# Kernel tuning notes

Measured on AMD Instinct MI355X. Metric: run time of the kernel, lower is better.

## Reference

```python
import jax, jax.numpy as jnp
import numpy as np

D_MODEL = 1024
NUM_HEADS = 16
THETA = 10000.0
BATCH = 2
SEQ = 2048


def _rope(x, pos, theta):
    # x: (b, h, l, d), pos: (l,)
    d = x.shape[-1]
    half = d // 2
    inv_freq = theta ** (-(jnp.arange(half, dtype=x.dtype) / half))  # theta^(-2k/d)
    ang = pos.astype(x.dtype)[:, None] * inv_freq[None, :]  # (l, half)
    cos, sin = jnp.cos(ang), jnp.sin(ang)
    x1, x2 = x[..., ::2], x[..., 1::2]
    r1 = x1 * cos - x2 * sin
    r2 = x1 * sin + x2 * cos
    return jnp.stack([r1, r2], axis=-1).reshape(x.shape)


def setup_inputs() -> dict:
    key = jax.random.key(0)
    k1, k2, k3 = jax.random.split(key, 3)
    x = jax.random.normal(k1, (BATCH, SEQ, D_MODEL), dtype=jnp.float32)
    W_kqv = jax.random.normal(k2, (3 * D_MODEL, D_MODEL), dtype=jnp.float32) * (1.0 / np.sqrt(D_MODEL))
    W_o = jax.random.normal(k3, (D_MODEL, D_MODEL), dtype=jnp.float32) * (1.0 / np.sqrt(D_MODEL))
    return {"x": x, "W_kqv": W_kqv, "W_o": W_o}


def reference(x, W_kqv, W_o):
    b, L, _ = x.shape
    h = NUM_HEADS
    d = D_MODEL // h
    kqv = x @ W_kqv.T  # (b, l, 3*d_model)
    K, Q, V = jnp.split(kqv, 3, axis=-1)  # chunk order in source: K, Q, V
    # (b, l, h*d) -> (b, h, l, d)
    Q = Q.reshape(b, L, h, d).transpose(0, 2, 1, 3)
    K = K.reshape(b, L, h, d).transpose(0, 2, 1, 3)
    V = V.reshape(b, L, h, d).transpose(0, 2, 1, 3)
    pos = jnp.arange(L)
    Q = _rope(Q, pos, THETA)
    K = _rope(K, pos, THETA)
    scores = jnp.einsum('bhqd,bhkd->bhqk', Q, K) / jnp.sqrt(jnp.asarray(d, x.dtype))
    causal = jnp.tril(jnp.ones((L, L), dtype=bool))
    scores = jnp.where(causal, scores, jnp.finfo(scores.dtype).min)
    probs = jax.nn.softmax(scores, axis=-1)
    out = jnp.einsum('bhqk,bhkd->bhqd', probs, V)
    out = out.transpose(0, 2, 1, 3).reshape(b, L, h * d)
    return out @ W_o.T
```

## Files before the change

kernel.cpp:

```cpp
#include <hip/hip_runtime.h>
#include <hip/hip_bf16.h>
#include <stdint.h>

#define BATCH 2
#define SEQ 2048
#define DMODEL 1024
#define NHEADS 16
#define HDIM 64
#define MROWS (BATCH*SEQ)
#define N3 (3*DMODEL)

typedef __attribute__((ext_vector_type(8))) __bf16 bf16x8;
typedef __attribute__((ext_vector_type(4))) float f32x4;

__device__ __forceinline__ ushort f2b(float f) {
  uint32_t u = __builtin_bit_cast(uint32_t, f);
  uint32_t r = (u + 0x7FFFu + ((u >> 16) & 1u)) >> 16;
  return (ushort)r;
}
__device__ __forceinline__ float b2f(ushort h) {
  return __builtin_bit_cast(float, (uint32_t)h << 16);
}
__device__ __forceinline__ float exp2_hw(float x) {
  float r;
  asm("v_exp_f32 %0, %1" : "=v"(r) : "v"(x));
  return r;
}
__device__ __forceinline__ uint32_t cvtpk(float a, float b) {
  uint32_t r;
  asm("v_cvt_pk_bf16_f32 %0, %1, %2" : "=v"(r) : "v"(a), "v"(b));
  return r;
}

__global__ void f2b3_kernel(const float* __restrict__ a, const float* __restrict__ b,
                            const float* __restrict__ c,
                            ushort* __restrict__ oa, ushort* __restrict__ ob,
                            ushort* __restrict__ oc, int na, int nb, int nc) {
  int i = blockIdx.x * blockDim.x + threadIdx.x;
  const float* src; ushort* dst; int off;
  if (i < na)           { src = a; dst = oa; off = i; }
  else if (i < na + nb) { src = b; dst = ob; off = i - na; }
  else if (i < na + nb + nc) { src = c; dst = oc; off = i - na - nb; }
  else return;
  float4 v = ((const float4*)src)[off];
  uint32_t lo = cvtpk(v.x, v.y), hi_ = cvtpk(v.z, v.w);
  ((uint2*)dst)[off] = make_uint2(lo, hi_);
}

template<int OUTF>
__global__ __launch_bounds__(256)
void gemm_bt(const ushort* __restrict__ A, const ushort* __restrict__ Bw,
             void* __restrict__ Cv, int M, int N, int K) {
  __shared__ __align__(16) ushort As[128*64];
  __shared__ __align__(16) ushort Bs[128*64];
  const int tid  = threadIdx.x;
  const int wid  = tid >> 6;
  const int lane = tid & 63;
  const int wr   = wid >> 1, wc = wid & 1;
  const int l16  = lane & 15, lhi = lane >> 4;
  const int nb   = N >> 7;
  const int brow = (blockIdx.x / nb) << 7;
  const int bcol = (blockIdx.x % nb) << 7;

  f32x4 acc[4][4] = {};

  for (int k0 = 0; k0 < K; k0 += 64) {
    __syncthreads();
#pragma unroll
    for (int it = 0; it < 4; ++it) {
      const int cb = (wid * 4 + it) * 64;
      const int ci = cb + lane;
      const int r  = ci >> 3;
      const int sl = (ci & 7) ^ (r & 7);
      const ushort* ga = A  + (size_t)(brow + r) * K + k0 + sl * 8;
      const ushort* gb = Bw + (size_t)(bcol + r) * K + k0 + sl * 8;
      __builtin_amdgcn_global_load_lds(
          (const __attribute__((address_space(1))) void*)ga,
          (__attribute__((address_space(3))) void*)(As + cb * 8), 16, 0, 0);
      __builtin_amdgcn_global_load_lds(
          (const __attribute__((address_space(1))) void*)gb,
          (__attribute__((address_space(3))) void*)(Bs + cb * 8), 16, 0, 0);
    }
    __syncthreads();

#pragma unroll
    for (int kk = 0; kk < 2; ++kk) {
      bf16x8 af[4], bfr[4];
#pragma unroll
      for (int m = 0; m < 4; ++m)
        af[m] = *(const bf16x8*)(As + (wr*64 + m*16 + l16)*64 + (((kk*4+lhi) ^ (l16 & 7)) * 8));
#pragma unroll
      for (int n = 0; n < 4; ++n)
        bfr[n] = *(const bf16x8*)(Bs + (wc*64 + n*16 + l16)*64 + (((kk*4+lhi) ^ (l16 & 7)) * 8));
#pragma unroll
      for (int m = 0; m < 4; ++m)
#pragma unroll
        for (int n = 0; n < 4; ++n)
          acc[m][n] = __builtin_amdgcn_mfma_f32_16x16x32_bf16(af[m], bfr[n], acc[m][n], 0, 0, 0);
    }
  }

#pragma unroll
  for (int m = 0; m < 4; ++m)
#pragma unroll
    for (int n = 0; n < 4; ++n)
#pragma unroll
      for (int r = 0; r < 4; ++r) {
        const int row = brow + wr*64 + m*16 + lhi*4 + r;
        const int col = bcol + wc*64 + n*16 + l16;
        if (OUTF) ((float*)Cv)[(size_t)row * N + col] = acc[m][n][r];
        else      ((ushort*)Cv)[(size_t)row * N + col] = f2b(acc[m][n][r]);
      }
}

__global__ __launch_bounds__(256)
void prep_kernel(const ushort* __restrict__ kqv,
                 ushort* __restrict__ qb, ushort* __restrict__ kb, ushort* __restrict__ vt) {
  __shared__ ushort tile[64][65];
  if (blockIdx.x < 1024) {
    int bid = blockIdx.x;
    int lt = bid & 31, bh = bid >> 5;
    int b = bh >> 4, h = bh & 15;
    int tid = threadIdx.x;
    int r = tid >> 2, cq = tid & 3;
    size_t gbase = ((size_t)(b * SEQ + lt * 64 + r)) * N3 + 2 * DMODEL + h * HDIM + cq * 16;
#pragma unroll
    for (int j = 0; j < 16; ++j) tile[r][cq * 16 + j] = kqv[gbase + j];
    __syncthreads();
    int d = tid >> 2;
    size_t obase = ((size_t)(bh * HDIM + d)) * SEQ + lt * 64 + cq * 16;
#pragma unroll
    for (int j = 0; j < 16; ++j) vt[obase + j] = tile[cq * 16 + j][d];
  } else {
    const float SC = 0.18033688011112042f;
    int idx = (blockIdx.x - 1024) * 256 + threadIdx.x;
    int i  = idx & 31;
    int h  = (idx >> 5) & 15;
    int bl = idx >> 9;
    int l  = bl & (SEQ - 1);
    int b  = bl >> 11;
    float inv = exp2f((float)i * -0.4152410118609203f);
    float ang = (float)l * inv;
    float s, c;
    sincosf(ang, &s, &c);
    size_t base = (size_t)bl * N3 + h * HDIM + 2 * i;
    uint32_t kp = *(const uint32_t*)(kqv + base);
    uint32_t qp = *(const uint32_t*)(kqv + base + DMODEL);
    float k1 = b2f((ushort)(kp & 0xffff)), k2 = b2f((ushort)(kp >> 16));
    float q1 = b2f((ushort)(qp & 0xffff)), q2 = b2f((ushort)(qp >> 16));
    float kr1 = k1 * c - k2 * s, kr2 = k1 * s + k2 * c;
    float qr1 = (q1 * c - q2 * s) * SC, qr2 = (q1 * s + q2 * c) * SC;
    size_t ob = ((size_t)(b * NHEADS + h) * SEQ + l) * HDIM + 2 * i;
    *(uint32_t*)(kb + ob) = cvtpk(kr1, kr2);
    *(uint32_t*)(qb + ob) = cvtpk(qr1, qr2);
  }
}

__global__ __launch_bounds__(256, 2)
void attn_kernel(const ushort* __restrict__ qb, const ushort* __restrict__ kb,
                 const ushort* __restrict__ vt, ushort* __restrict__ ao) {
  __shared__ __align__(16) ushort Kbuf[3][4096];
  __shared__ __align__(16) ushort Vbuf[3][4096];
  __shared__ __align__(16) ushort plds[4][1024];
  const int bid = blockIdx.x;
  const int bh = bid & 31;
  const int p  = bid >> 5;
  const int qtA = p, qtB = 31 - p;

  const int wid = threadIdx.x >> 6, lane = threadIdx.x & 63;
  const int l16 = lane & 15, lhi = lane >> 4;
  const int r0A = qtA * 64 + wid * 16;
  const int r0B = qtB * 64 + wid * 16;

  const ushort* Q  = qb + (size_t)bh * SEQ * HDIM;
  const ushort* Kp = kb + (size_t)bh * SEQ * HDIM;
  const ushort* Vp = vt + (size_t)bh * HDIM * SEQ;

  bf16x8 qfA[2], qfB[2];
#pragma unroll
  for (int kc = 0; kc < 2; ++kc) {
    qfA[kc] = *(const bf16x8*)(Q + (size_t)(r0A + l16) * HDIM + kc * 32 + lhi * 8);
    qfB[kc] = *(const bf16x8*)(Q + (size_t)(r0B + l16) * HDIM + kc * 32 + lhi * 8);
  }

  float mqA = -3.0e38f, lsA = 0.0f, mqB = -3.0e38f, lsB = 0.0f;
  f32x4 oA[4] = {}, oB[4] = {};

  char* pbase = (char*)&plds[wid][0];
  const int swz = (l16 & 7) << 4;

  auto STAGE = [&](int buf, int kt) {
    ushort* kd = &Kbuf[buf][0];
    ushort* vd = &Vbuf[buf][0];
    const ushort* kg = Kp + (size_t)kt * 64 * HDIM;
    const ushort* vg = Vp + kt * 64;
#pragma unroll
    for (int it = 0; it < 2; ++it) {
      const int cb = it * 256 + wid * 64;
      const int ci = cb + lane;
      const int row = ci >> 3;
      const int sl  = (ci & 7) ^ (row & 7);
      __builtin_amdgcn_global_load_lds(
          (const __attribute__((address_space(1))) void*)(kg + row * HDIM + sl * 8),
          (__attribute__((address_space(3))) void*)(kd + cb * 8), 16, 0, 0);
      __builtin_amdgcn_global_load_lds(
          (const __attribute__((address_space(1))) void*)(vg + (size_t)row * SEQ + sl * 8),
          (__attribute__((address_space(3))) void*)(vd + cb * 8), 16, 0, 0);
    }
  };

  auto BODY = [&](const char* kc_, const char* vc_, bf16x8 (&qf)[2],
                  float& mq, float& lsq, f32x4 (&o)[4], int r0, int qt, int kt) {
    f32x4 s[4];
#pragma unroll
    for (int n = 0; n < 4; ++n) {
      const int kvr = n * 16 + l16;
      bf16x8 kf0 = *(const bf16x8*)(kc_ + kvr*128 + ((lhi     ^ (kvr&7)) * 16));
      bf16x8 kf1 = *(const bf16x8*)(kc_ + kvr*128 + (((4+lhi) ^ (kvr&7)) * 16));
      f32x4 z = 0.0f;
      z = __builtin_amdgcn_mfma_f32_16x16x32_bf16(kf0, qf[0], z, 0, 0, 0);
      z = __builtin_amdgcn_mfma_f32_16x16x32_bf16(kf1, qf[1], z, 0, 0, 0);
      s[n] = z;
    }
    if (kt == qt) {
#pragma unroll
      for (int n = 0; n < 4; ++n)
#pragma unroll
        for (int r = 0; r < 4; ++r)
          if (kt*64 + n*16 + lhi*4 + r > r0 + l16) s[n][r] = -3.0e38f;
    }
    float t0 = fmaxf(fmaxf(s[0][0], s[0][1]), fmaxf(s[0][2], s[0][3]));
    float t1 = fmaxf(fmaxf(s[1][0], s[1][1]), fmaxf(s[1][2], s[1][3]));
    float t2 = fmaxf(fmaxf(s[2][0], s[2][1]), fmaxf(s[2][2], s[2][3]));
    float t3 = fmaxf(fmaxf(s[3][0], s[3][1]), fmaxf(s[3][2], s[3][3]));
    float pmx = fmaxf(fmaxf(t0, t1), fmaxf(t2, t3));
    pmx = fmaxf(pmx, __shfl_xor(pmx, 16));
    pmx = fmaxf(pmx, __shfl_xor(pmx, 32));

    if (!__all(pmx <= mq)) {
      float mn = fmaxf(mq, pmx);
      float alpha = exp2_hw(mq - mn);
      mq = mn;
      lsq *= alpha;
      float alphaT[4];
#pragma unroll
      for (int r = 0; r < 4; ++r)
        alphaT[r] = __shfl(alpha, lhi * 4 + r);
#pragma unroll
      for (int f = 0; f < 4; ++f)
#pragma unroll
        for (int r = 0; r < 4; ++r)
          o[f][r] *= alphaT[r];
    }

    float ps = 0.0f;
#pragma unroll
    for (int n = 0; n < 4; ++n)
#pragma unroll
      for (int r = 0; r < 4; ++r) {
        float pv = exp2_hw(s[n][r] - mq);
        s[n][r] = pv;
        ps += pv;
      }
    ps += __shfl_xor(ps, 16);
    ps += __shfl_xor(ps, 32);
    lsq += ps;

#pragma unroll
    for (int n = 0; n < 4; ++n) {
      uint32_t w0 = cvtpk(s[n][0], s[n][1]);
      uint32_t w1 = cvtpk(s[n][2], s[n][3]);
      int kvloc = n*16 + lhi*4;
      *(uint32_t*)(pbase + ((l16*128 + kvloc*2) ^ swz))       = w0;
      *(uint32_t*)(pbase + ((l16*128 + (kvloc+2)*2) ^ swz))   = w1;
    }
    bf16x8 pa0 = *(const bf16x8*)(pbase + ((l16*128 + 0*64 + lhi*16) ^ swz));
    bf16x8 pa1 = *(const bf16x8*)(pbase + ((l16*128 + 1*64 + lhi*16) ^ swz));

#pragma unroll
    for (int f = 0; f < 4; ++f) {
      const int dr = f * 16 + l16;
      bf16x8 vf0 = *(const bf16x8*)(vc_ + dr*128 + ((lhi     ^ (dr&7)) * 16));
      bf16x8 vf1 = *(const bf16x8*)(vc_ + dr*128 + (((4+lhi) ^ (dr&7)) * 16));
      o[f] = __builtin_amdgcn_mfma_f32_16x16x32_bf16(pa0, vf0, o[f], 0, 0, 0);
      o[f] = __builtin_amdgcn_mfma_f32_16x16x32_bf16(pa1, vf1, o[f], 0, 0, 0);
    }
  };

  STAGE(0, 0);
  STAGE(1, 1);

  for (int kt = 0; kt <= qtB; ++kt) {
    if (kt < qtB) asm volatile("s_waitcnt vmcnt(4)" ::: "memory");
    else          asm volatile("s_waitcnt vmcnt(0)" ::: "memory");
    __builtin_amdgcn_s_barrier();
    __builtin_amdgcn_sched_barrier(0);

    if (kt + 2 <= qtB) STAGE((kt + 2) % 3, kt + 2);

    const char* kc_ = (const char*)&Kbuf[kt % 3][0];
    const char* vc_ = (const char*)&Vbuf[kt % 3][0];
    BODY(kc_, vc_, qfB, mqB, lsB, oB, r0B, qtB, kt);
    if (kt <= qtA)
      BODY(kc_, vc_, qfA, mqA, lsA, oA, r0A, qtA, kt);

    __builtin_amdgcn_sched_barrier(0);
  }

  const int b = bh >> 4, h = bh & 15;
  float invA = 1.0f / lsA, invB = 1.0f / lsB;
#pragma unroll
  for (int r = 0; r < 4; ++r) {
    float wA = __shfl(invA, lhi * 4 + r);
    float wB = __shfl(invB, lhi * 4 + r);
    size_t baseA = ((size_t)(b * SEQ + r0A + lhi*4 + r)) * DMODEL + h * HDIM + l16;
    size_t baseB = ((size_t)(b * SEQ + r0B + lhi*4 + r)) * DMODEL + h * HDIM + l16;
#pragma unroll
    for (int f = 0; f < 4; ++f) {
      ao[baseA + f*16] = f2b(oA[f][r] * wA);
      ao[baseB + f*16] = f2b(oB[f][r] * wB);
    }
  }
}

extern "C" void kernel_launch(void* const* d_in, const int* in_sizes, int n_in,
                              void* d_out, int out_size, void* d_ws, size_t ws_size,
                              hipStream_t stream) {
  const float* x    = (const float*)d_in[0];
  const float* wkqv = (const float*)d_in[1];
  const float* wo   = (const float*)d_in[2];
  float* out = (float*)d_out;

  ushort* xb   = (ushort*)d_ws;
  ushort* wkb  = xb  + (size_t)MROWS * DMODEL;
  ushort* wob  = wkb + (size_t)N3 * DMODEL;
  ushort* kqv  = wob + (size_t)DMODEL * DMODEL;
  ushort* qb   = kqv + (size_t)MROWS * N3;
  ushort* kb   = qb  + (size_t)MROWS * DMODEL;
  ushort* vt   = kb  + (size_t)MROWS * DMODEL;
  ushort* attn = xb;

  int nx = MROWS * DMODEL / 4, nw = N3 * DMODEL / 4, no = DMODEL * DMODEL / 4;
  f2b3_kernel<<<(nx + nw + no) / 256, 256, 0, stream>>>(x, wkqv, wo, xb, wkb, wob, nx, nw, no);

  gemm_bt<0><<<(MROWS/128) * (N3/128), 256, 0, stream>>>(xb, wkb, (void*)kqv, MROWS, N3, DMODEL);

  prep_kernel<<<1024 + (MROWS * NHEADS * 32) / 256, 256, 0, stream>>>(kqv, qb, kb, vt);

  attn_kernel<<<512, 256, 0, stream>>>(qb, kb, vt, attn);

  gemm_bt<1><<<(MROWS/128) * (DMODEL/128), 256, 0, stream>>>(attn, wob, (void*)out, MROWS, DMODEL, DMODEL);
}
```

Baseline: 120.1 us.

## Use 256x256-tile double-buffered GEMM with direct global-to-LDS loads for QKV projection

Result: slower. 123.3 us (+2.6%).

```diff
diff --git a/kernel.cpp b/kernel.cpp
--- a/kernel.cpp
+++ b/kernel.cpp
@@ -45,6 +45,136 @@
   float4 v = ((const float4*)src)[off];
   uint32_t lo = cvtpk(v.x, v.y), hi_ = cvtpk(v.z, v.w);
   ((uint2*)dst)[off] = make_uint2(lo, hi_);
+}
+
+__global__ __launch_bounds__(512)
+void gemm256_bt(const ushort* __restrict__ A, const ushort* __restrict__ Bw,
+                ushort* __restrict__ C, int M, int N, int K) {
+  __shared__ __align__(16) ushort As[2][256*64];
+  __shared__ __align__(16) ushort Bs[2][256*64];
+  const int tid  = threadIdx.x;
+  const int wid  = tid >> 6;
+  const int lane = tid & 63;
+  const int wr   = wid >> 2, wc = wid & 3;
+  const int l16  = lane & 15, lhi = lane >> 4;
+  const int nb   = N >> 8;
+  const int brow = (blockIdx.x / nb) << 8;
+  const int bcol = (blockIdx.x % nb) << 8;
+  const int sw   = l16 & 7;
+  const int nt   = K >> 6;
+
+  f32x4 acc[8][4] = {};
+
+  auto STAGE_A = [&](int buf, int t) {
+#pragma unroll
+    for (int j = 0; j < 4; ++j) {
+      const int cb  = (wid * 4 + j) * 64;
+      const int ci  = cb + lane;
+      const int row = ci >> 3;
+      const int sl  = (ci & 7) ^ (row & 7);
+      __builtin_amdgcn_global_load_lds(
+          (const __attribute__((address_space(1))) void*)(A + (size_t)(brow + row) * K + t * 64 + sl * 8),
+          (__attribute__((address_space(3))) void*)(&As[buf][0] + cb * 8), 16, 0, 0);
+    }
+  };
+  auto STAGE_B = [&](int buf, int t) {
+#pragma unroll
+    for (int j = 0; j < 4; ++j) {
+      const int cb  = (wid * 4 + j) * 64;
+      const int ci  = cb + lane;
+      const int row = ci >> 3;
+      const int sl  = (ci & 7) ^ (row & 7);
+      __builtin_amdgcn_global_load_lds(
+          (const __attribute__((address_space(1))) void*)(Bw + (size_t)(bcol + row) * K + t * 64 + sl * 8),
+          (__attribute__((address_space(3))) void*)(&Bs[buf][0] + cb * 8), 16, 0, 0);
+    }
+  };
+
+  STAGE_A(0, 0);
+  STAGE_B(0, 0);
+
+  for (int t = 0; t < nt; ++t) {
+    const int nxt = (t + 1) & 1;
+    const int cur = t & 1;
+    if (t + 1 < nt) {
+      STAGE_A(nxt, t + 1);
+      asm volatile("s_waitcnt vmcnt(4)" ::: "memory");
+    } else {
+      asm volatile("s_waitcnt vmcnt(0)" ::: "memory");
+    }
+    __builtin_amdgcn_s_barrier();
+    __builtin_amdgcn_sched_barrier(0);
+
+    const ushort* as_ = &As[cur][0];
+    const ushort* bs_ = &Bs[cur][0];
+
+    bf16x8 af[4], bfr[4];
+#pragma unroll
+    for (int m = 0; m < 4; ++m)
+      af[m] = *(const bf16x8*)(as_ + (wr*128 + m*16 + l16)*64 + ((lhi ^ sw) * 8));
+#pragma unroll
+    for (int n = 0; n < 4; ++n)
+      bfr[n] = *(const bf16x8*)(bs_ + (wc*64 + n*16 + l16)*64 + ((lhi ^ sw) * 8));
+    __builtin_amdgcn_s_setprio(1);
+#pragma unroll
+    for (int m = 0; m < 4; ++m)
+#pragma unroll
+      for (int n = 0; n < 4; ++n)
+        acc[m][n] = __builtin_amdgcn_mfma_f32_16x16x32_bf16(af[m], bfr[n], acc[m][n], 0, 0, 0);
+    __builtin_amdgcn_s_setprio(0);
+#pragma unroll
+    for (int m = 0; m < 4; ++m)
+      af[m] = *(const bf16x8*)(as_ + (wr*128 + (m+4)*16 + l16)*64 + ((lhi ^ sw) * 8));
+    __builtin_amdgcn_s_setprio(1);
+#pragma unroll
+    for (int m = 0; m < 4; ++m)
+#pragma unroll
+      for (int n = 0; n < 4; ++n)
+        acc[m+4][n] = __builtin_amdgcn_mfma_f32_16x16x32_bf16(af[m], bfr[n], acc[m+4][n], 0, 0, 0);
+    __builtin_amdgcn_s_setprio(0);
+
+    if (t + 1 < nt) STAGE_B(nxt, t + 1);
+    __builtin_amdgcn_s_barrier();
+    __builtin_amdgcn_sched_barrier(0);
+
+#pragma unroll
+    for (int m = 0; m < 4; ++m)
+      af[m] = *(const bf16x8*)(as_ + (wr*128 + m*16 + l16)*64 + (((4+lhi) ^ sw) * 8));
+#pragma unroll
+    for (int n = 0; n < 4; ++n)
+      bfr[n] = *(const bf16x8*)(bs_ + (wc*64 + n*16 + l16)*64 + (((4+lhi) ^ sw) * 8));
+    __builtin_amdgcn_s_setprio(1);
+#pragma unroll
+    for (int m = 0; m < 4; ++m)
+#pragma unroll
+      for (int n = 0; n < 4; ++n)
+        acc[m][n] = __builtin_amdgcn_mfma_f32_16x16x32_bf16(af[m], bfr[n], acc[m][n], 0, 0, 0);
+    __builtin_amdgcn_s_setprio(0);
+#pragma unroll
+    for (int m = 0; m < 4; ++m)
+      af[m] = *(const bf16x8*)(as_ + (wr*128 + (m+4)*16 + l16)*64 + (((4+lhi) ^ sw) * 8));
+    __builtin_amdgcn_s_setprio(1);
+#pragma unroll
+    for (int m = 0; m < 4; ++m)
+#pragma unroll
+      for (int n = 0; n < 4; ++n)
+        acc[m+4][n] = __builtin_amdgcn_mfma_f32_16x16x32_bf16(af[m], bfr[n], acc[m+4][n], 0, 0, 0);
+    __builtin_amdgcn_s_setprio(0);
+
+    __builtin_amdgcn_s_barrier();
+    __builtin_amdgcn_sched_barrier(0);
+  }
+
+#pragma unroll
+  for (int m = 0; m < 8; ++m)
+#pragma unroll
+    for (int n = 0; n < 4; ++n)
+#pragma unroll
+      for (int r = 0; r < 4; ++r) {
+        const int row = brow + wr*128 + m*16 + lhi*4 + r;
+        const int col = bcol + wc*64 + n*16 + l16;
+        C[(size_t)row * N + col] = f2b(acc[m][n][r]);
+      }
 }
 
 template<int OUTF>
@@ -343,7 +473,7 @@
   int nx = MROWS * DMODEL / 4, nw = N3 * DMODEL / 4, no = DMODEL * DMODEL / 4;
   f2b3_kernel<<<(nx + nw + no) / 256, 256, 0, stream>>>(x, wkqv, wo, xb, wkb, wob, nx, nw, no);
 
-  gemm_bt<0><<<(MROWS/128) * (N3/128), 256, 0, stream>>>(xb, wkb, (void*)kqv, MROWS, N3, DMODEL);
+  gemm256_bt<<<(MROWS/256) * (N3/256), 512, 0, stream>>>(xb, wkb, kqv, MROWS, N3, DMODEL);
 
   prep_kernel<<<1024 + (MROWS * NHEADS * 32) / 256, 256, 0, stream>>>(kqv, qb, kb, vt);
 
```

## Double-buffer LDS tiles in GEMM with split A/B prefetch and MFMA priority

Applied to the files above, without the earlier changes.

After: 136.1 us. 13.3% more time.

```diff
diff --git a/kernel.cpp b/kernel.cpp
--- a/kernel.cpp
+++ b/kernel.cpp
@@ -51,8 +51,8 @@
 __global__ __launch_bounds__(256)
 void gemm_bt(const ushort* __restrict__ A, const ushort* __restrict__ Bw,
              void* __restrict__ Cv, int M, int N, int K) {
-  __shared__ __align__(16) ushort As[128*64];
-  __shared__ __align__(16) ushort Bs[128*64];
+  __shared__ __align__(16) ushort As[2][128*64];
+  __shared__ __align__(16) ushort Bs[2][128*64];
   const int tid  = threadIdx.x;
   const int wid  = tid >> 6;
   const int lane = tid & 63;
@@ -61,43 +61,89 @@
   const int nb   = N >> 7;
   const int brow = (blockIdx.x / nb) << 7;
   const int bcol = (blockIdx.x % nb) << 7;
+  const int sw   = l16 & 7;
+  const int nt   = K >> 6;
 
   f32x4 acc[4][4] = {};
 
-  for (int k0 = 0; k0 < K; k0 += 64) {
-    __syncthreads();
-#pragma unroll
-    for (int it = 0; it < 4; ++it) {
-      const int cb = (wid * 4 + it) * 64;
-      const int ci = cb + lane;
-      const int r  = ci >> 3;
-      const int sl = (ci & 7) ^ (r & 7);
-      const ushort* ga = A  + (size_t)(brow + r) * K + k0 + sl * 8;
-      const ushort* gb = Bw + (size_t)(bcol + r) * K + k0 + sl * 8;
+  auto STAGE_A = [&](int buf, int t) {
+#pragma unroll
+    for (int j = 0; j < 4; ++j) {
+      const int cb  = (wid * 4 + j) * 64;
+      const int ci  = cb + lane;
+      const int row = ci >> 3;
+      const int sl  = (ci & 7) ^ (row & 7);
       __builtin_amdgcn_global_load_lds(
-          (const __attribute__((address_space(1))) void*)ga,
-          (__attribute__((address_space(3))) void*)(As + cb * 8), 16, 0, 0);
+          (const __attribute__((address_space(1))) void*)(A + (size_t)(brow + row) * K + t * 64 + sl * 8),
+          (__attribute__((address_space(3))) void*)(&As[buf][0] + cb * 8), 16, 0, 0);
+    }
+  };
+  auto STAGE_B = [&](int buf, int t) {
+#pragma unroll
+    for (int j = 0; j < 4; ++j) {
+      const int cb  = (wid * 4 + j) * 64;
+      const int ci  = cb + lane;
+      const int row = ci >> 3;
+      const int sl  = (ci & 7) ^ (row & 7);
       __builtin_amdgcn_global_load_lds(
-          (const __attribute__((address_space(1))) void*)gb,
-          (__attribute__((address_space(3))) void*)(Bs + cb * 8), 16, 0, 0);
-    }
-    __syncthreads();
-
-#pragma unroll
-    for (int kk = 0; kk < 2; ++kk) {
-      bf16x8 af[4], bfr[4];
-#pragma unroll
-      for (int m = 0; m < 4; ++m)
-        af[m] = *(const bf16x8*)(As + (wr*64 + m*16 + l16)*64 + (((kk*4+lhi) ^ (l16 & 7)) * 8));
+          (const __attribute__((address_space(1))) void*)(Bw + (size_t)(bcol + row) * K + t * 64 + sl * 8),
+          (__attribute__((address_space(3))) void*)(&Bs[buf][0] + cb * 8), 16, 0, 0);
+    }
+  };
+
+  STAGE_A(0, 0);
+  STAGE_B(0, 0);
+
+  for (int t = 0; t < nt; ++t) {
+    const int cur = t & 1;
+    const int nxt = cur ^ 1;
+    if (t + 1 < nt) {
+      STAGE_A(nxt, t + 1);
+      asm volatile("s_waitcnt vmcnt(4)" ::: "memory");
+    } else {
+      asm volatile("s_waitcnt vmcnt(0)" ::: "memory");
+    }
+    __builtin_amdgcn_s_barrier();
+    __builtin_amdgcn_sched_barrier(0);
+
+    const ushort* as_ = &As[cur][0];
+    const ushort* bs_ = &Bs[cur][0];
+
+    bf16x8 af[4], bfr[4];
+#pragma unroll
+    for (int m = 0; m < 4; ++m)
+      af[m] = *(const bf16x8*)(as_ + (wr*64 + m*16 + l16)*64 + ((lhi ^ sw) * 8));
+#pragma unroll
+    for (int n = 0; n < 4; ++n)
+      bfr[n] = *(const bf16x8*)(bs_ + (wc*64 + n*16 + l16)*64 + ((lhi ^ sw) * 8));
+    __builtin_amdgcn_s_setprio(1);
+#pragma unroll
+    for (int m = 0; m < 4; ++m)
 #pragma unroll
       for (int n = 0; n < 4; ++n)
-        bfr[n] = *(const bf16x8*)(Bs + (wc*64 + n*16 + l16)*64 + (((kk*4+lhi) ^ (l16 & 7)) * 8));
-#pragma unroll
-      for (int m = 0; m < 4; ++m)
-#pragma unroll
-        for (int n = 0; n < 4; ++n)
-          acc[m][n] = __builtin_amdgcn_mfma_f32_16x16x32_bf16(af[m], bfr[n], acc[m][n], 0, 0, 0);
-    }
+        acc[m][n] = __builtin_amdgcn_mfma_f32_16x16x32_bf16(af[m], bfr[n], acc[m][n], 0, 0, 0);
+    __builtin_amdgcn_s_setprio(0);
+
+    if (t + 1 < nt) STAGE_B(nxt, t + 1);
+    __builtin_amdgcn_s_barrier();
+    __builtin_amdgcn_sched_barrier(0);
+
+#pragma unroll
+    for (int m = 0; m < 4; ++m)
+      af[m] = *(const bf16x8*)(as_ + (wr*64 + m*16 + l16)*64 + (((4+lhi) ^ sw) * 8));
+#pragma unroll
+    for (int n = 0; n < 4; ++n)
+      bfr[n] = *(const bf16x8*)(bs_ + (wc*64 + n*16 + l16)*64 + (((4+lhi) ^ sw) * 8));
+    __builtin_amdgcn_s_setprio(1);
+#pragma unroll
+    for (int m = 0; m < 4; ++m)
+#pragma unroll
+      for (int n = 0; n < 4; ++n)
+        acc[m][n] = __builtin_amdgcn_mfma_f32_16x16x32_bf16(af[m], bfr[n], acc[m][n], 0, 0, 0);
+    __builtin_amdgcn_s_setprio(0);
+
+    __builtin_amdgcn_s_barrier();
+    __builtin_amdgcn_sched_barrier(0);
   }
 
 #pragma unroll
```
